# Kernel tuning notes

Measured on AMD Instinct MI355X. Metric: run time of the kernel, lower is better.

Reference implementation:

```python
import jax, jax.numpy as jnp
import numpy as np

PRE_NMS_THRESH = 0.05
PRE_NMS_TOP_N = 200
NMS_THRESH = 0.5
FPN_POST_NMS_TOP_N = 100
MIN_SIZE = 0.0
NUM_CLASSES = 2
C = NUM_CLASSES - 1
NB = 2
STRIDES = (8, 16, 32, 64, 128)
HS = (100, 50, 25, 13, 7)
WS = (128, 64, 32, 16, 8)
IMG_H, IMG_W = 800, 1024
MAXV = 8  # max #vertices of quad-clipped-by-quad polygon


def _shoelace_fixed(V, n):
    # area of polygon stored in fixed buffer V[MAXV,2] with n valid vertices
    a = jnp.asarray(0.0, V.dtype)
    for k in range(MAXV):
        nxt = jnp.where(jnp.equal(k, n - 1), 0, k + 1)
        term = V[k, 0] * V[nxt, 1] - V[nxt, 0] * V[k, 1]
        a = a + jnp.where(k < n, term, 0.0)
    return 0.5 * jnp.abs(a)


def _quad_area(Q):  # Q: [4,2]
    x, y = Q[:, 0], Q[:, 1]
    return 0.5 * jnp.abs(jnp.sum(x * jnp.roll(y, -1) - jnp.roll(x, -1) * y))


def _clip_halfplane(V, n, p1, p2, orient):
    # Sutherland-Hodgman clip of polygon (V,n) against directed edge p1->p2
    d = p2 - p1

    def side(p):
        return orient * (d[0] * (p[1] - p1[1]) - d[1] * (p[0] - p1[0]))

    out = jnp.zeros((MAXV, 2), V.dtype)
    cnt = jnp.int32(0)
    for k in range(MAXV):
        cur = V[k]
        prev = V[jnp.where(jnp.equal(k, 0), n - 1, k - 1)]
        sc = side(cur)
        sp = side(prev)
        cur_in = sc >= 0.0
        prev_in = sp >= 0.0
        denom = sp - sc
        t = sp / jnp.where(jnp.abs(denom) > 1e-9, denom, 1e-9)
        ip = prev + t * (cur - prev)
        valid = k < n
        emit_ip = valid & (cur_in != prev_in)
        out = jnp.where(emit_ip, out.at[cnt].set(ip, mode='drop'), out)
        cnt = cnt + emit_ip.astype(jnp.int32)
        emit_cur = valid & cur_in
        out = jnp.where(emit_cur, out.at[cnt].set(cur, mode='drop'), out)
        cnt = cnt + emit_cur.astype(jnp.int32)
    return out, cnt


def _poly_inter_area(A, B):  # A,B: [4,2] convex quads
    sB = jnp.sum(B[:, 0] * jnp.roll(B[:, 1], -1) - jnp.roll(B[:, 0], -1) * B[:, 1])
    orient = jnp.where(sB >= 0.0, 1.0, -1.0)
    V = jnp.zeros((MAXV, 2), A.dtype).at[:4].set(A)
    n = jnp.int32(4)
    for e in range(4):
        V, n = _clip_halfplane(V, n, B[e], B[(e + 1) % 4], orient)
    return _shoelace_fixed(V, n)


def _process_level(loc, cls_l, reg_l, image_sizes):
    Nb, Cc, H, W = cls_l.shape
    # (N,C,H,W) -> (N,HW*C) with index = (h*W+w)*C + c (matches permute/reshape)
    scores = jax.nn.sigmoid(cls_l.transpose(0, 2, 3, 1).reshape(Nb, H * W * Cc))
    cand = scores > PRE_NMS_THRESH
    masked = jnp.where(cand, scores, 0.0)
    k = min(PRE_NMS_TOP_N, H * W * Cc)
    vals, idx = jax.lax.top_k(masked, k)
    loc_idx = idx // Cc
    labels = idx % Cc + 1
    regr = reg_l.transpose(0, 2, 3, 1).reshape(Nb, H * W, 8)
    reg_g = jnp.take_along_axis(regr, loc_idx[..., None], axis=1)  # [Nb,k,8]
    loc_g = loc[loc_idx]  # [Nb,k,2]
    poly = jnp.tile(loc_g, (1, 1, 4)) - reg_g  # (x-r0, y-r1, ..., x-r6, y-r7)
    hh = image_sizes[:, 0].astype(poly.dtype)[:, None, None]
    ww = image_sizes[:, 1].astype(poly.dtype)[:, None, None]
    xs = jnp.clip(poly[..., 0::2], 0.0, ww - 1.0)
    ys = jnp.clip(poly[..., 1::2], 0.0, hh - 1.0)
    poly = jnp.stack([xs, ys], axis=-1).reshape(Nb, k, 8)
    valid = vals > PRE_NMS_THRESH
    bw = xs.max(-1) - xs.min(-1)
    bh = ys.max(-1) - ys.min(-1)
    valid = valid & (bw >= MIN_SIZE) & (bh >= MIN_SIZE)
    sc = jnp.where(valid, jnp.sqrt(vals), 0.0)
    return poly, sc, labels, valid


def _nms_single(poly, scores, labels, valid):
    T = scores.shape[0]
    order = jnp.argsort(-scores)
    poly = poly[order]
    scores = scores[order]
    labels = labels[order]
    valid = valid[order]
    quads = poly.reshape(T, 4, 2)

    def pairwise_iou(q):
        inter = jax.vmap(jax.vmap(_poly_inter_area, (None, 0)), (0, None))(q, q)
        areas = jax.vmap(_quad_area)(q)
        union = areas[:, None] + areas[None, :] - inter
        return inter / jnp.maximum(union, 1e-9)

    # IoU only feeds boolean suppression decisions -> no gradient flows through it
    iou = jax.lax.stop_gradient(pairwise_iou(quads))
    ar = jnp.arange(T)

    def body(i, keep):
        sup = (iou[i] > NMS_THRESH) & (ar > i)
        return jnp.where(keep[i], keep & ~sup, keep)

    keep = jax.lax.stop_gradient(jax.lax.fori_loop(0, T, body, valid))
    final = jnp.where(keep, scores, -1.0)
    top_s, top_i = jax.lax.top_k(final, FPN_POST_NMS_TOP_N)
    ok = top_s > 0.0
    return poly[top_i], jnp.where(ok, top_s, 0.0), labels[top_i], ok


def _forward(locs, clss, regs, image_sizes):
    parts = [_process_level(l, c, r, image_sizes) for l, c, r in zip(locs, clss, regs)]
    poly = jnp.concatenate([p[0] for p in parts], axis=1)
    sc = jnp.concatenate([p[1] for p in parts], axis=1)
    lab = jnp.concatenate([p[2] for p in parts], axis=1)
    val = jnp.concatenate([p[3] for p in parts], axis=1)
    return jax.vmap(_nms_single)(poly, sc, lab, val)


def setup_inputs() -> dict:
    key = jax.random.key(0)
    inp = {}
    k = key
    for i, (h, w, s) in enumerate(zip(HS, WS, STRIDES)):
        k, k1, k2, k3 = jax.random.split(k, 4)
        sx = jnp.arange(w, dtype=jnp.float32) * s + s // 2
        sy = jnp.arange(h, dtype=jnp.float32) * s + s // 2
        yy, xx = jnp.meshgrid(sy, sx, indexing='ij')
        inp[f'locations_l{i}'] = jnp.stack([xx.reshape(-1), yy.reshape(-1)], axis=1)
        inp[f'box_cls_l{i}'] = jax.random.normal(k1, (NB, C, h, w), dtype=jnp.float32)
        inp[f'box_reg_l{i}'] = jax.random.normal(k2, (NB, 8, h, w), dtype=jnp.float32) * (2.0 * s)
        inp[f'centerness_l{i}'] = jax.random.normal(k3, (NB, 1, h, w), dtype=jnp.float32)
    inp['image_sizes'] = jnp.array([[IMG_H, IMG_W]] * NB, dtype=jnp.int32)
    return inp


def reference(locations_l0, locations_l1, locations_l2, locations_l3, locations_l4,
              box_cls_l0, box_cls_l1, box_cls_l2, box_cls_l3, box_cls_l4,
              box_reg_l0, box_reg_l1, box_reg_l2, box_reg_l3, box_reg_l4,
              centerness_l0, centerness_l1, centerness_l2, centerness_l3, centerness_l4,
              image_sizes):
    # centerness is accepted but unused, matching the original module's forward
    locs = [locations_l0, locations_l1, locations_l2, locations_l3, locations_l4]
    clss = [box_cls_l0, box_cls_l1, box_cls_l2, box_cls_l3, box_cls_l4]
    regs = [box_reg_l0, box_reg_l1, box_reg_l2, box_reg_l3, box_reg_l4]
    boxes, scores, labels, valid = _forward(locs, clss, regs, image_sizes)
    return boxes, scores, labels, valid
```

## Files before the change

### kernel.cpp

```cpp
#include <hip/hip_runtime.h>

#pragma clang fp contract(off)

#define T_CAND 856
#define NW 14
#define NSH 16
#define HSTR 513

__device__ const int d_HW[5]  = {12800, 3200, 800, 208, 56};
__device__ const int d_K[5]   = {200, 200, 200, 200, 56};
__device__ const int d_OFF[5] = {0, 200, 400, 600, 800};

struct LevelPtrs {
  const float* loc[5];
  const float* cls[5];
  const float* reg[5];
  const int*   img;
};

__device__ __forceinline__ unsigned long long readlane64(unsigned long long v, int lane) {
  const unsigned lo = (unsigned)__builtin_amdgcn_readlane((int)(unsigned)(v & 0xFFFFFFFFULL), lane);
  const unsigned hi = (unsigned)__builtin_amdgcn_readlane((int)(unsigned)(v >> 32), lane);
  return ((unsigned long long)hi << 32) | lo;
}
__device__ __forceinline__ unsigned long long rfl64(unsigned long long v) {
  const unsigned lo = (unsigned)__builtin_amdgcn_readfirstlane((int)(unsigned)(v & 0xFFFFFFFFULL));
  const unsigned hi = (unsigned)__builtin_amdgcn_readfirstlane((int)(unsigned)(v >> 32));
  return ((unsigned long long)hi << 32) | lo;
}

__global__ __launch_bounds__(1024) void topk_kernel(LevelPtrs P,
    float* __restrict__ candPoly, float* __restrict__ candSc, unsigned* __restrict__ candValid) {
  __shared__ unsigned hist[NSH * HSTR];
  __shared__ unsigned histT[512];
  __shared__ __align__(16) unsigned long long gbuf[1024];
  __shared__ float mcache[12800];
  __shared__ int gcount;
  __shared__ int cutB;
  const int blk = blockIdx.x;
  const int b = blk / 5, l = blk % 5;
  const int HW = d_HW[l], K = d_K[l], OFF = d_OFF[l];
  const float* cls = P.cls[l] + (size_t)b * HW;
  const float* reg = P.reg[l] + (size_t)b * 8 * HW;
  const float* loc = P.loc[l];
  const int tid = threadIdx.x;
  const int wave = tid >> 6, lane = tid & 63;

  for (int t = tid; t < NSH * HSTR; t += 1024) hist[t] = 0u;
  if (tid == 0) gcount = 0;
  __syncthreads();

  const int sh = (tid >> 2) & (NSH - 1);
  for (int idx = tid; idx < HW; idx += 1024) {
    const float x = cls[idx];
    const float s = (float)(1.0 / (1.0 + exp(-(double)x)));
    const float m = (s > 0.05f) ? s : 0.0f;
    mcache[idx] = m;
    atomicAdd(&hist[sh * HSTR + (__float_as_uint(m) >> 21)], 1u);
  }
  __syncthreads();
  for (int t = tid; t < 512; t += 1024) {
    unsigned sum = 0;
#pragma unroll
    for (int h = 0; h < NSH; ++h) sum += hist[h * HSTR + t];
    histT[t] = sum;
  }
  __syncthreads();
  if (wave == 0) {
    const int t0 = lane * 8;
    int h[8], loc8[8];
#pragma unroll
    for (int k = 0; k < 8; ++k) h[k] = (int)histT[t0 + k];
    int run = 0;
#pragma unroll
    for (int k = 7; k >= 0; --k) { run += h[k]; loc8[k] = run; }
    int v = run;
#pragma unroll
    for (int d = 1; d < 64; d <<= 1) {
      const int u = __shfl_down(v, d);
      if (lane + d < 64) v += u;
    }
    const int excl = v - run;
    int cand = -1;
#pragma unroll
    for (int k = 7; k >= 0; --k)
      if (cand < 0 && excl + loc8[k] >= K) cand = t0 + k;
    const unsigned long long bal = __ballot(cand >= 0);
    const int hi = 63 - __builtin_clzll(bal);
    const int cb = __shfl(cand, hi);
    if (lane == 0) cutB = cb;
  }
  __syncthreads();

  const int cb = cutB;
  for (int idx = tid; idx < HW; idx += 1024) {
    const unsigned kb = __float_as_uint(mcache[idx]);
    if ((int)(kb >> 21) >= cb) {
      const int pos = atomicAdd(&gcount, 1);
      if (pos < 1024)
        gbuf[pos] = ((unsigned long long)kb << 32)
                  | (unsigned long long)(0xFFFFFFFFu - (unsigned)idx);
    }
  }
  __syncthreads();
  const int G = min(gcount, 1024);
  if (tid < 4 && G + tid < 1024) gbuf[G + tid] = 0ULL;
  __syncthreads();

  if (tid < G) {
    const unsigned long long my = gbuf[tid];
    const int G4 = (G + 3) & ~3;
    int rank = 0;
    const ulonglong2* g2 = (const ulonglong2*)gbuf;
    for (int j = 0; j < G4 / 2; j += 2) {
      const ulonglong2 a = g2[j], c = g2[j + 1];
      rank += (a.x > my) ? 1 : 0;
      rank += (a.y > my) ? 1 : 0;
      rank += (c.x > my) ? 1 : 0;
      rank += (c.y > my) ? 1 : 0;
    }
    if (rank < K) {
      const float val = __uint_as_float((unsigned)(my >> 32));
      const int idx = (int)(0xFFFFFFFFu - (unsigned)(my & 0xFFFFFFFFULL));
      const float hh = (float)P.img[b * 2 + 0];
      const float ww = (float)P.img[b * 2 + 1];
      const float xmax = ww - 1.0f, ymax = hh - 1.0f;
      const float lx = loc[idx * 2 + 0], ly = loc[idx * 2 + 1];
      const int go = b * T_CAND + OFF + rank;
#pragma unroll
      for (int q = 0; q < 4; ++q) {
        const float rx = reg[(2 * q + 0) * HW + idx];
        const float ry = reg[(2 * q + 1) * HW + idx];
        const float pxv = fminf(fmaxf(lx - rx, 0.0f), xmax);
        const float pyv = fminf(fmaxf(ly - ry, 0.0f), ymax);
        candPoly[go * 8 + 2 * q + 0] = pxv;
        candPoly[go * 8 + 2 * q + 1] = pyv;
      }
      const bool v = (val > 0.05f);
      candSc[go]    = v ? sqrtf(val) : 0.0f;
      candValid[go] = v ? 1u : 0u;
    }
  }
}

__global__ __launch_bounds__(1024) void sort_kernel(
    const float* __restrict__ candPoly, const float* __restrict__ candSc,
    const unsigned* __restrict__ candValid,
    float* __restrict__ sPoly, float* __restrict__ sSc, unsigned* __restrict__ sValid,
    float* __restrict__ sAABB) {
  __shared__ __align__(16) unsigned long long key[T_CAND];
  const int b = blockIdx.x, tid = threadIdx.x;
  float sc = 0.0f;
  if (tid < T_CAND) {
    sc = candSc[b * T_CAND + tid];
    key[tid] = ((unsigned long long)__float_as_uint(sc) << 32)
             | (unsigned long long)(0xFFFFFFFFu - (unsigned)tid);
  }
  __syncthreads();
  if (tid < T_CAND) {
    const unsigned long long my = key[tid];
    int rank = 0;
    const ulonglong2* k2 = (const ulonglong2*)key;
    for (int j = 0; j < T_CAND / 2; j += 2) {
      const ulonglong2 a = k2[j], c = k2[j + 1];
      rank += (a.x > my) ? 1 : 0;
      rank += (a.y > my) ? 1 : 0;
      rank += (c.x > my) ? 1 : 0;
      rank += (c.y > my) ? 1 : 0;
    }
    sSc[b * T_CAND + rank]    = sc;
    sValid[b * T_CAND + rank] = candValid[b * T_CAND + tid];
    const float4* src = (const float4*)(candPoly + (size_t)(b * T_CAND + tid) * 8);
    const float4 s0 = src[0], s1 = src[1];
    float4* dst = (float4*)(sPoly + (size_t)(b * T_CAND + rank) * 8);
    dst[0] = s0;
    dst[1] = s1;
    float4 bb;
    bb.x = fminf(fminf(s0.x, s0.z), fminf(s1.x, s1.z));
    bb.y = fminf(fminf(s0.y, s0.w), fminf(s1.y, s1.w));
    bb.z = fmaxf(fmaxf(s0.x, s0.z), fmaxf(s1.x, s1.z));
    bb.w = fmaxf(fmaxf(s0.y, s0.w), fmaxf(s1.y, s1.w));
    *(float4*)(sAABB + (size_t)(b * T_CAND + rank) * 4) = bb;
  }
}

__global__ __launch_bounds__(256) void tile_clip_kernel(
    const float* __restrict__ sPoly, const unsigned* __restrict__ sValid,
    const float* __restrict__ sAABB, unsigned long long* __restrict__ MT) {
  __shared__ float VX[2][8][256];
  __shared__ float VY[2][8][256];
  __shared__ __align__(16) float4 ra[64];
  __shared__ unsigned rv[64];
  __shared__ unsigned long long cw[64];
  __shared__ unsigned long long ow[64];
  __shared__ unsigned pl[4096];
  __shared__ int cnt;
  const int b = blockIdx.y;
  int it = 0, rem = blockIdx.x;
  while (rem >= NW - it) { rem -= NW - it; ++it; }
  const int jt = it + rem;
  const int tid = threadIdx.x;
  const int wave = tid >> 6, lane = tid & 63;

  if (tid == 0) cnt = 0;
  if (tid < 64) {
    const int row = it * 64 + tid;
    const int rc = row < T_CAND ? row : (T_CAND - 1);
    ra[tid] = *(const float4*)(sAABB + (size_t)(b * T_CAND + rc) * 4);
    rv[tid] = (row < T_CAND) ? sValid[b * T_CAND + row] : 0u;
    ow[tid] = 0ULL;
  }
  __syncthreads();

  const int j = jt * 64 + lane;
  const int jcl = j < T_CAND ? j : (T_CAND - 1);
  const float4 jb = *(const float4*)(sAABB + (size_t)(b * T_CAND + jcl) * 4);
  const bool jv = (j < T_CAND) && (sValid[b * T_CAND + jcl] != 0u);
#pragma unroll
  for (int k = 0; k < 16; ++k) {
    const int r = wave * 16 + k;
    const int irow = it * 64 + r;
    const float4 ib = ra[r];
    const bool iv = rv[r] != 0u;
    const bool ov = !(ib.z < jb.x || jb.z < ib.x || ib.w < jb.y || jb.w < ib.y);
    const bool pred = iv && jv && (j > irow) && ov;
    const unsigned long long w = __ballot(pred);
    if (lane == 0) cw[r] = w;
  }
  __syncthreads();
  if (tid < 64) {
    unsigned long long w = cw[tid];
    const int c = __popcll(w);
    int off = c ? atomicAdd(&cnt, c) : 0;
    while (w) {
      const int jo = (int)__builtin_ctzll(w);
      w &= w - 1;
      pl[off++] = ((unsigned)tid << 6) | (unsigned)jo;
    }
  }
  __syncthreads();
  const int total = cnt;
  for (int p = tid; p < total; p += 256) {
    const unsigned pk = pl[p];
    const int io = (int)(pk >> 6), jo = (int)(pk & 63u);
    const int i = it * 64 + io, jj = jt * 64 + jo;
    const float4* Ap4 = (const float4*)(sPoly + (size_t)(b * T_CAND + i) * 8);
    const float4 a01 = Ap4[0], a23 = Ap4[1];
    const float ax0 = a01.x, ay0 = a01.y, ax1 = a01.z, ay1 = a01.w,
                ax2 = a23.x, ay2 = a23.y, ax3 = a23.z, ay3 = a23.w;
    const float4* Bp4 = (const float4*)(sPoly + (size_t)(b * T_CAND + jj) * 8);
    const float4 b01 = Bp4[0], b23 = Bp4[1];
    const float bx0 = b01.x, by0 = b01.y, bx1 = b01.z, by1 = b01.w,
                bx2 = b23.x, by2 = b23.y, bx3 = b23.z, by3 = b23.w;
    float sB = bx0 * by1 - bx1 * by0;
    sB += bx1 * by2 - bx2 * by1;
    sB += bx2 * by3 - bx3 * by2;
    sB += bx3 * by0 - bx0 * by3;
    const float orient = (sB >= 0.0f) ? 1.0f : -1.0f;

    VX[0][0][tid] = ax0; VY[0][0][tid] = ay0;
    VX[0][1][tid] = ax1; VY[0][1][tid] = ay1;
    VX[0][2][tid] = ax2; VY[0][2][tid] = ay2;
    VX[0][3][tid] = ax3; VY[0][3][tid] = ay3;
    int n = 4;
    const float bex[5] = {bx0, bx1, bx2, bx3, bx0};
    const float bey[5] = {by0, by1, by2, by3, by0};
#pragma unroll
    for (int e = 0; e < 4; ++e) {
      const int src = e & 1, dst = src ^ 1;
      const float p1x = bex[e], p1y = bey[e];
      const float dx = bex[e + 1] - p1x, dy = bey[e + 1] - p1y;
      int cn = 0;
      int pidx = n - 1;
      pidx = pidx < 0 ? 0 : (pidx > 7 ? 7 : pidx);
      float px = VX[src][pidx][tid], py = VY[src][pidx][tid];
      float sp = orient * (dx * (py - p1y) - dy * (px - p1x));
      for (int k = 0; k < 8; ++k) {
        if (k >= n) break;
        const float cx = VX[src][k][tid], cy = VY[src][k][tid];
        const float sc2 = orient * (dx * (cy - p1y) - dy * (cx - p1x));
        const bool cin = (sc2 >= 0.0f), pin = (sp >= 0.0f);
        const float denom = sp - sc2;
        const float dd = (fabsf(denom) > 1e-9f) ? denom : 1e-9f;
        const float t = sp / dd;
        const float ipx = px + t * (cx - px);
        const float ipy = py + t * (cy - py);
        const bool e1 = (cin != pin);
        if (e1 && cn < 8) { VX[dst][cn][tid] = ipx; VY[dst][cn][tid] = ipy; }
        cn += e1 ? 1 : 0;
        if (cin && cn < 8) { VX[dst][cn][tid] = cx; VY[dst][cn][tid] = cy; }
        cn += cin ? 1 : 0;
        px = cx; py = cy; sp = sc2;
      }
      n = cn;
    }
    float a = 0.0f;
    for (int k = 0; k < 8; ++k) {
      if (k >= n) break;
      const int nxt = (k == n - 1) ? 0 : ((k + 1 > 7) ? 7 : (k + 1));
      const float xk = VX[0][k][tid], yk = VY[0][k][tid];
      const float xn = VX[0][nxt][tid], yn = VY[0][nxt][tid];
      a += xk * yn - xn * yk;
    }
    const float inter = 0.5f * fabsf(a);
    float aA = ax0 * ay1 - ax1 * ay0;
    aA += ax1 * ay2 - ax2 * ay1;
    aA += ax2 * ay3 - ax3 * ay2;
    aA += ax3 * ay0 - ax0 * ay3;
    const float areaA = 0.5f * fabsf(aA);
    const float areaB = 0.5f * fabsf(sB);
    const float uni = areaA + areaB - inter;
    const float iou = inter / fmaxf(uni, 1e-9f);
    if (iou > 0.5f) atomicOr(&ow[io], 1ULL << jo);
  }
  __syncthreads();
  if (tid < 64) {
    const int row = it * 64 + tid;
    if (row < T_CAND) MT[((size_t)b * NW + jt) * T_CAND + row] = ow[tid];
  }
}

__global__ __launch_bounds__(1024) void nms_resolve_emit_kernel(
    const unsigned long long* __restrict__ MT, const unsigned* __restrict__ sValid,
    const float* __restrict__ sPoly, const float* __restrict__ sSc, float* __restrict__ out) {
  __shared__ __align__(16) unsigned long long mt[NW * T_CAND];
  __shared__ unsigned long long vb[16];
  __shared__ unsigned long long kw[NW];
  const int b = blockIdx.x;
  const int tid = threadIdx.x;
  const int wave = tid >> 6, lane = tid & 63;

  {
    const ulonglong2* g2 = (const ulonglong2*)(MT + (size_t)b * NW * T_CAND);
    ulonglong2* l2 = (ulonglong2*)mt;
    for (int t = tid; t < NW * T_CAND / 2; t += 1024) l2[t] = g2[t];
  }
  if (wave < NW) {
    const int idx = wave * 64 + lane;
    const bool v = (idx < T_CAND) && (sValid[b * T_CAND + idx] != 0u);
    const unsigned long long ball = __ballot(v);
    if (lane == 0) vb[wave] = ball;
  }
  __syncthreads();

  if (wave == 0) {
    unsigned long long kwreg = 0ULL;
    for (int q = 0; q < NW; ++q) {
      const unsigned long long* col = &mt[q * T_CAND];
      const int nrow = q * 64 + lane;
      const unsigned long long sup = col[nrow < T_CAND ? nrow : (T_CAND - 1)];
      unsigned long long acc = 0ULL;
      for (int wp = 0; wp < q; ++wp) {
        const unsigned long long row = col[wp * 64 + lane];
        const unsigned long long kword = readlane64(kwreg, wp);
        acc |= ((kword >> lane) & 1ULL) ? row : 0ULL;
      }
#pragma unroll
      for (int m = 1; m < 64; m <<= 1)
        acc |= (unsigned long long)__shfl_xor((long long)acc, m, 64);
      const unsigned long long S = rfl64(acc);
      const unsigned long long validq = rfl64(vb[q]);
      unsigned long long alive = validq & ~S;
      const unsigned long long suppr = __ballot(sup != 0ULL);
      unsigned long long rem = alive & suppr;
      while (rem) {
        const int s = (int)__builtin_ctzll(rem);
        rem &= rem - 1;
        if ((alive >> s) & 1ULL) {
          alive &= ~readlane64(sup, s);
          rem &= alive;
        }
      }
      if (lane == q) kwreg = alive;
    }
    if (lane < NW) kw[lane] = kwreg;
  }
  __syncthreads();

  if (tid < 100) {
    const int o = tid;
    int totalKeep = 0;
    for (int w = 0; w < NW; ++w) totalKeep += __popcll(kw[w]);
    const bool kept = o < totalKeep;
    int idx = 0;
    if (kept) {
      int r = o, w = 0;
      unsigned long long word = 0ULL;
      for (; w < NW; ++w) {
        word = kw[w];
        const int c = __popcll(word);
        if (r < c) break;
        r -= c;
      }
      for (int p = 0; p < r; ++p) word &= word - 1;
      idx = w * 64 + (__ffsll(word) - 1);
    } else {
      int r = o - totalKeep, w = 0;
      unsigned long long word = 0ULL;
      for (; w < NW; ++w) {
        const unsigned long long mk = (w == NW - 1) ? ((1ULL << (T_CAND - 64 * (NW - 1))) - 1ULL)
                                                    : ~0ULL;
        word = (~kw[w]) & mk;
        const int c = __popcll(word);
        if (r < c) break;
        r -= c;
      }
      for (int p = 0; p < r; ++p) word &= word - 1;
      idx = w * 64 + (__ffsll(word) - 1);
    }
    const float4* pp = (const float4*)(sPoly + (size_t)(b * T_CAND + idx) * 8);
    float4* ob2 = (float4*)(out + (size_t)b * 800 + (size_t)o * 8);
    ob2[0] = pp[0];
    ob2[1] = pp[1];
    out[1600 + b * 100 + o] = kept ? sSc[b * T_CAND + idx] : 0.0f;
    out[1800 + b * 100 + o] = 1.0f;
    out[2000 + b * 100 + o] = kept ? 1.0f : 0.0f;
  }
}

extern "C" void kernel_launch(void* const* d_in, const int* in_sizes, int n_in,
                              void* d_out, int out_size, void* d_ws, size_t ws_size,
                              hipStream_t stream) {
  (void)n_in; (void)out_size; (void)ws_size;
  LevelPtrs P;
  const bool interleaved = (in_sizes[2] == 204800);
  for (int l = 0; l < 5; ++l) {
    if (interleaved) {
      P.loc[l] = (const float*)d_in[4 * l + 0];
      P.cls[l] = (const float*)d_in[4 * l + 1];
      P.reg[l] = (const float*)d_in[4 * l + 2];
    } else {
      P.loc[l] = (const float*)d_in[l];
      P.cls[l] = (const float*)d_in[5 + l];
      P.reg[l] = (const float*)d_in[10 + l];
    }
  }
  P.img = (const int*)d_in[20];

  char* ws = (char*)d_ws;
  float*    candPoly  = (float*)(ws + 0);
  float*    candSc    = (float*)(ws + 54784);
  unsigned* candValid = (unsigned*)(ws + 61632);
  float*    sPoly     = (float*)(ws + 68480);
  float*    sSc       = (float*)(ws + 123264);
  unsigned* sValid    = (unsigned*)(ws + 130112);
  unsigned long long* MT = (unsigned long long*)(ws + 136960);
  float*    sAABB     = (float*)(ws + 328704);

  topk_kernel<<<dim3(10), dim3(1024), 0, stream>>>(P, candPoly, candSc, candValid);
  sort_kernel<<<dim3(2), dim3(1024), 0, stream>>>(candPoly, candSc, candValid,
                                                  sPoly, sSc, sValid, sAABB);
  tile_clip_kernel<<<dim3((NW * (NW + 1)) / 2, 2), dim3(256), 0, stream>>>(sPoly, sValid,
                                                                           sAABB, MT);
  nms_resolve_emit_kernel<<<dim3(2), dim3(1024), 0, stream>>>(MT, sValid, sPoly, sSc,
                                                              (float*)d_out);
}
```

Baseline: 91.81 us.

## Split pair filtering from polygon clipping and clip in registers over global pair list

The fused tile kernel is split in two. One kernel builds a global list of AABB-overlapping pairs with an atomic counter, and a separate grid-stride kernel clips each pair, which balances work across many more blocks than the uneven per-tile lists did. The Sutherland-Hodgman clip now keeps vertices in registers through predicated selects instead of shared-memory arrays, and IoU bits go straight to global MT with atomicOr. The cost is an extra kernel launch, global atomics, and more register pressure from the unrolled select chains.

```diff
diff --git a/kernel.cpp b/kernel.cpp
--- a/kernel.cpp
+++ b/kernel.cpp
@@ -30,7 +30,8 @@
 }
 
 __global__ __launch_bounds__(1024) void topk_kernel(LevelPtrs P,
-    float* __restrict__ candPoly, float* __restrict__ candSc, unsigned* __restrict__ candValid) {
+    float* __restrict__ candPoly, float* __restrict__ candSc, unsigned* __restrict__ candValid,
+    unsigned* __restrict__ pairCount) {
   __shared__ unsigned hist[NSH * HSTR];
   __shared__ unsigned histT[512];
   __shared__ __align__(16) unsigned long long gbuf[1024];
@@ -46,6 +47,7 @@
   const int tid = threadIdx.x;
   const int wave = tid >> 6, lane = tid & 63;
 
+  if (blk == 0 && tid == 0) *pairCount = 0u;
   for (int t = tid; t < NSH * HSTR; t += 1024) hist[t] = 0u;
   if (tid == 0) gcount = 0;
   __syncthreads();
@@ -184,17 +186,16 @@
   }
 }
 
-__global__ __launch_bounds__(256) void tile_clip_kernel(
-    const float* __restrict__ sPoly, const unsigned* __restrict__ sValid,
-    const float* __restrict__ sAABB, unsigned long long* __restrict__ MT) {
-  __shared__ float VX[2][8][256];
-  __shared__ float VY[2][8][256];
+__global__ __launch_bounds__(256) void pairs_kernel(
+    const unsigned* __restrict__ sValid, const float* __restrict__ sAABB,
+    unsigned long long* __restrict__ MT, unsigned* __restrict__ pairList,
+    unsigned* __restrict__ pairCount) {
   __shared__ __align__(16) float4 ra[64];
   __shared__ unsigned rv[64];
   __shared__ unsigned long long cw[64];
-  __shared__ unsigned long long ow[64];
-  __shared__ unsigned pl[4096];
-  __shared__ int cnt;
+  __shared__ int rowoff[64];
+  __shared__ int lcnt;
+  __shared__ int gbase;
   const int b = blockIdx.y;
   int it = 0, rem = blockIdx.x;
   while (rem >= NW - it) { rem -= NW - it; ++it; }
@@ -202,13 +203,13 @@
   const int tid = threadIdx.x;
   const int wave = tid >> 6, lane = tid & 63;
 
-  if (tid == 0) cnt = 0;
+  if (tid == 0) lcnt = 0;
   if (tid < 64) {
     const int row = it * 64 + tid;
     const int rc = row < T_CAND ? row : (T_CAND - 1);
     ra[tid] = *(const float4*)(sAABB + (size_t)(b * T_CAND + rc) * 4);
     rv[tid] = (row < T_CAND) ? sValid[b * T_CAND + row] : 0u;
-    ow[tid] = 0ULL;
+    if (row < T_CAND) MT[((size_t)b * NW + jt) * T_CAND + row] = 0ULL;
   }
   __syncthreads();
 
@@ -229,26 +230,37 @@
   }
   __syncthreads();
   if (tid < 64) {
+    const int c = __popcll(cw[tid]);
+    rowoff[tid] = c ? atomicAdd(&lcnt, c) : 0;
+  }
+  __syncthreads();
+  if (tid == 0) gbase = lcnt ? (int)atomicAdd(pairCount, (unsigned)lcnt) : 0;
+  __syncthreads();
+  if (tid < 64) {
     unsigned long long w = cw[tid];
-    const int c = __popcll(w);
-    int off = c ? atomicAdd(&cnt, c) : 0;
+    unsigned off = (unsigned)(gbase + rowoff[tid]);
+    const int iRow = it * 64 + tid;
     while (w) {
       const int jo = (int)__builtin_ctzll(w);
       w &= w - 1;
-      pl[off++] = ((unsigned)tid << 6) | (unsigned)jo;
-    }
-  }
-  __syncthreads();
-  const int total = cnt;
-  for (int p = tid; p < total; p += 256) {
-    const unsigned pk = pl[p];
-    const int io = (int)(pk >> 6), jo = (int)(pk & 63u);
-    const int i = it * 64 + io, jj = jt * 64 + jo;
+      pairList[off++] = ((unsigned)b << 20) | ((unsigned)iRow << 10) | (unsigned)(jt * 64 + jo);
+    }
+  }
+}
+
+__global__ __launch_bounds__(256) void clip_kernel(
+    const unsigned* __restrict__ pairList, const unsigned* __restrict__ pairCount,
+    const float* __restrict__ sPoly, unsigned long long* __restrict__ MT) {
+  const int tid = threadIdx.x;
+  const unsigned count = *pairCount;
+  for (unsigned t0 = blockIdx.x * 256 + tid; t0 < count; t0 += gridDim.x * 256) {
+    const unsigned pk = pairList[t0];
+    const int b = (pk >> 20) & 1, i = (pk >> 10) & 1023, j = pk & 1023;
     const float4* Ap4 = (const float4*)(sPoly + (size_t)(b * T_CAND + i) * 8);
     const float4 a01 = Ap4[0], a23 = Ap4[1];
     const float ax0 = a01.x, ay0 = a01.y, ax1 = a01.z, ay1 = a01.w,
                 ax2 = a23.x, ay2 = a23.y, ax3 = a23.z, ay3 = a23.w;
-    const float4* Bp4 = (const float4*)(sPoly + (size_t)(b * T_CAND + jj) * 8);
+    const float4* Bp4 = (const float4*)(sPoly + (size_t)(b * T_CAND + j) * 8);
     const float4 b01 = Bp4[0], b23 = Bp4[1];
     const float bx0 = b01.x, by0 = b01.y, bx1 = b01.z, by1 = b01.w,
                 bx2 = b23.x, by2 = b23.y, bx3 = b23.z, by3 = b23.w;
@@ -257,66 +269,96 @@
     sB += bx2 * by3 - bx3 * by2;
     sB += bx3 * by0 - bx0 * by3;
     const float orient = (sB >= 0.0f) ? 1.0f : -1.0f;
-
-    VX[0][0][tid] = ax0; VY[0][0][tid] = ay0;
-    VX[0][1][tid] = ax1; VY[0][1][tid] = ay1;
-    VX[0][2][tid] = ax2; VY[0][2][tid] = ay2;
-    VX[0][3][tid] = ax3; VY[0][3][tid] = ay3;
-    int n = 4;
-    const float bex[5] = {bx0, bx1, bx2, bx3, bx0};
-    const float bey[5] = {by0, by1, by2, by3, by0};
-#pragma unroll
-    for (int e = 0; e < 4; ++e) {
-      const int src = e & 1, dst = src ^ 1;
-      const float p1x = bex[e], p1y = bey[e];
-      const float dx = bex[e + 1] - p1x, dy = bey[e + 1] - p1y;
-      int cn = 0;
-      int pidx = n - 1;
-      pidx = pidx < 0 ? 0 : (pidx > 7 ? 7 : pidx);
-      float px = VX[src][pidx][tid], py = VY[src][pidx][tid];
-      float sp = orient * (dx * (py - p1y) - dy * (px - p1x));
-      for (int k = 0; k < 8; ++k) {
-        if (k >= n) break;
-        const float cx = VX[src][k][tid], cy = VY[src][k][tid];
-        const float sc2 = orient * (dx * (cy - p1y) - dy * (cx - p1x));
-        const bool cin = (sc2 >= 0.0f), pin = (sp >= 0.0f);
-        const float denom = sp - sc2;
-        const float dd = (fabsf(denom) > 1e-9f) ? denom : 1e-9f;
-        const float t = sp / dd;
-        const float ipx = px + t * (cx - px);
-        const float ipy = py + t * (cy - py);
-        const bool e1 = (cin != pin);
-        if (e1 && cn < 8) { VX[dst][cn][tid] = ipx; VY[dst][cn][tid] = ipy; }
-        cn += e1 ? 1 : 0;
-        if (cin && cn < 8) { VX[dst][cn][tid] = cx; VY[dst][cn][tid] = cy; }
-        cn += cin ? 1 : 0;
-        px = cx; py = cy; sp = sc2;
-      }
-      n = cn;
-    }
-    float a = 0.0f;
-    for (int k = 0; k < 8; ++k) {
-      if (k >= n) break;
-      const int nxt = (k == n - 1) ? 0 : ((k + 1 > 7) ? 7 : (k + 1));
-      const float xk = VX[0][k][tid], yk = VY[0][k][tid];
-      const float xn = VX[0][nxt][tid], yn = VY[0][nxt][tid];
-      a += xk * yn - xn * yk;
-    }
-    const float inter = 0.5f * fabsf(a);
     float aA = ax0 * ay1 - ax1 * ay0;
     aA += ax1 * ay2 - ax2 * ay1;
     aA += ax2 * ay3 - ax3 * ay2;
     aA += ax3 * ay0 - ax0 * ay3;
+
+    float s0x = ax0, s0y = ay0, s1x = ax1, s1y = ay1,
+          s2x = ax2, s2y = ay2, s3x = ax3, s3y = ay3,
+          s4x = 0.f, s4y = 0.f, s5x = 0.f, s5y = 0.f,
+          s6x = 0.f, s6y = 0.f, s7x = 0.f, s7y = 0.f;
+    int n = 4;
+    float lastx = ax3, lasty = ay3;
+    const float bex[5] = {bx0, bx1, bx2, bx3, bx0};
+    const float bey[5] = {by0, by1, by2, by3, by0};
+
+#define PUSH(w_, vx_, vy_)                                              \
+    {                                                                   \
+      const bool w__ = (w_);                                            \
+      const float vx__ = (vx_), vy__ = (vy_);                           \
+      t0x = (w__ && cnt == 0) ? vx__ : t0x; t0y = (w__ && cnt == 0) ? vy__ : t0y; \
+      t1x = (w__ && cnt == 1) ? vx__ : t1x; t1y = (w__ && cnt == 1) ? vy__ : t1y; \
+      t2x = (w__ && cnt == 2) ? vx__ : t2x; t2y = (w__ && cnt == 2) ? vy__ : t2y; \
+      t3x = (w__ && cnt == 3) ? vx__ : t3x; t3y = (w__ && cnt == 3) ? vy__ : t3y; \
+      t4x = (w__ && cnt == 4) ? vx__ : t4x; t4y = (w__ && cnt == 4) ? vy__ : t4y; \
+      t5x = (w__ && cnt == 5) ? vx__ : t5x; t5y = (w__ && cnt == 5) ? vy__ : t5y; \
+      t6x = (w__ && cnt == 6) ? vx__ : t6x; t6y = (w__ && cnt == 6) ? vy__ : t6y; \
+      t7x = (w__ && cnt == 7) ? vx__ : t7x; t7y = (w__ && cnt == 7) ? vy__ : t7y; \
+      nlx = (w__ && cnt < 8) ? vx__ : nlx;  nly = (w__ && cnt < 8) ? vy__ : nly;  \
+      cnt += w__ ? 1 : 0;                                               \
+    }
+
+#define CLIP_K(k_, sx_, sy_)                                            \
+    {                                                                   \
+      const bool act = (k_) < n;                                        \
+      const float cx = sx_, cy = sy_;                                   \
+      const float sc2 = orient * (dx * (cy - p1y) - dy * (cx - p1x));   \
+      const bool cin = (sc2 >= 0.0f), pin = (sp >= 0.0f);               \
+      const float den = sp - sc2;                                       \
+      const float dd = (fabsf(den) > 1e-9f) ? den : 1e-9f;              \
+      const float tt = sp / dd;                                         \
+      const float ipx = px + tt * (cx - px);                            \
+      const float ipy = py + tt * (cy - py);                            \
+      PUSH(act && (cin != pin), ipx, ipy);                              \
+      PUSH(act && cin, cx, cy);                                         \
+      px = cx; py = cy; sp = sc2;                                       \
+    }
+
+#pragma unroll
+    for (int e = 0; e < 4; ++e) {
+      const float p1x = bex[e], p1y = bey[e];
+      const float dx = bex[e + 1] - p1x, dy = bey[e + 1] - p1y;
+      float t0x = 0.f, t0y = 0.f, t1x = 0.f, t1y = 0.f, t2x = 0.f, t2y = 0.f,
+            t3x = 0.f, t3y = 0.f, t4x = 0.f, t4y = 0.f, t5x = 0.f, t5y = 0.f,
+            t6x = 0.f, t6y = 0.f, t7x = 0.f, t7y = 0.f;
+      float nlx = lastx, nly = lasty;
+      int cnt = 0;
+      float px = lastx, py = lasty;
+      float sp = orient * (dx * (py - p1y) - dy * (px - p1x));
+      CLIP_K(0, s0x, s0y) CLIP_K(1, s1x, s1y) CLIP_K(2, s2x, s2y) CLIP_K(3, s3x, s3y)
+      CLIP_K(4, s4x, s4y) CLIP_K(5, s5x, s5y) CLIP_K(6, s6x, s6y) CLIP_K(7, s7x, s7y)
+      s0x = t0x; s0y = t0y; s1x = t1x; s1y = t1y; s2x = t2x; s2y = t2y;
+      s3x = t3x; s3y = t3y; s4x = t4x; s4y = t4y; s5x = t5x; s5y = t5y;
+      s6x = t6x; s6y = t6y; s7x = t7x; s7y = t7y;
+      lastx = nlx; lasty = nly;
+      n = cnt;
+    }
+#undef CLIP_K
+#undef PUSH
+
+    float a = 0.0f;
+#define SHOE(k_, xk_, yk_, xn_, yn_)                                    \
+    {                                                                   \
+      const bool act = (k_) < n;                                        \
+      const bool wrap = (k_) == n - 1;                                  \
+      const float xn = wrap ? s0x : (xn_);                              \
+      const float yn = wrap ? s0y : (yn_);                              \
+      const float term = (xk_) * yn - xn * (yk_);                       \
+      a += act ? term : 0.0f;                                           \
+    }
+    SHOE(0, s0x, s0y, s1x, s1y) SHOE(1, s1x, s1y, s2x, s2y)
+    SHOE(2, s2x, s2y, s3x, s3y) SHOE(3, s3x, s3y, s4x, s4y)
+    SHOE(4, s4x, s4y, s5x, s5y) SHOE(5, s5x, s5y, s6x, s6y)
+    SHOE(6, s6x, s6y, s7x, s7y) SHOE(7, s7x, s7y, s7x, s7y)
+#undef SHOE
+    const float inter = 0.5f * fabsf(a);
     const float areaA = 0.5f * fabsf(aA);
     const float areaB = 0.5f * fabsf(sB);
     const float uni = areaA + areaB - inter;
     const float iou = inter / fmaxf(uni, 1e-9f);
-    if (iou > 0.5f) atomicOr(&ow[io], 1ULL << jo);
-  }
-  __syncthreads();
-  if (tid < 64) {
-    const int row = it * 64 + tid;
-    if (row < T_CAND) MT[((size_t)b * NW + jt) * T_CAND + row] = ow[tid];
+    if (iou > 0.5f)
+      atomicOr(&MT[((size_t)b * NW + (j >> 6)) * T_CAND + i], 1ULL << (j & 63));
   }
 }
 
@@ -446,12 +488,15 @@
   unsigned* sValid    = (unsigned*)(ws + 130112);
   unsigned long long* MT = (unsigned long long*)(ws + 136960);
   float*    sAABB     = (float*)(ws + 328704);
-
-  topk_kernel<<<dim3(10), dim3(1024), 0, stream>>>(P, candPoly, candSc, candValid);
+  unsigned* pairCount = (unsigned*)(ws + 356096);
+  unsigned* pairList  = (unsigned*)(ws + 356112);
+
+  topk_kernel<<<dim3(10), dim3(1024), 0, stream>>>(P, candPoly, candSc, candValid, pairCount);
   sort_kernel<<<dim3(2), dim3(1024), 0, stream>>>(candPoly, candSc, candValid,
                                                   sPoly, sSc, sValid, sAABB);
-  tile_clip_kernel<<<dim3((NW * (NW + 1)) / 2, 2), dim3(256), 0, stream>>>(sPoly, sValid,
-                                                                           sAABB, MT);
+  pairs_kernel<<<dim3((NW * (NW + 1)) / 2, 2), dim3(256), 0, stream>>>(sValid, sAABB, MT,
+                                                                       pairList, pairCount);
+  clip_kernel<<<dim3(512), dim3(256), 0, stream>>>(pairList, pairCount, sPoly, MT);
   nms_resolve_emit_kernel<<<dim3(2), dim3(1024), 0, stream>>>(MT, sValid, sPoly, sSc,
                                                               (float*)d_out);
 }
```

Result: faster. 74.75 us (-18.6%).
